# Kernel optimization log

Hardware: AMD Instinct MI355X
Metric: run time of the kernel (lower is better)

## Reference

```python
import jax, jax.numpy as jnp
import numpy as np

N, CIN, CH, W = 512, 128, 256, 8

def _refpad(x):
    # ReflectionPad2d(1) on NCHW
    return jnp.pad(x, ((0, 0), (0, 0), (1, 1), (1, 1)), mode='reflect')

def _conv(x, w, b):
    # x: NCHW padded, w: OIHW 3x3, VALID conv back to 8x8
    y = jax.lax.conv_general_dilated(x, w, (1, 1), 'VALID',
                                     dimension_numbers=('NCHW', 'OIHW', 'NCHW'))
    return y + b[None, :, None, None]

def setup_inputs() -> dict:
    key = jax.random.key(0)
    ks = jax.random.split(key, 24)
    s_in = 1.0 / np.sqrt(CIN * 9)
    s_h = 1.0 / np.sqrt(CH * 9)
    d = {
        'x': jax.random.normal(ks[0], (N, CIN, W, W), jnp.float32),
        'hidden_state': jax.random.normal(ks[1], (N, 2, CH, W, W), jnp.float32),
    }
    names_i = ['w_ii', 'w_if', 'w_ig', 'w_io']
    names_h = ['w_hi', 'w_hf', 'w_hg', 'w_ho']
    for j, nm in enumerate(names_i):
        d[nm] = jax.random.uniform(ks[2 + j], (CH, CIN, 3, 3), jnp.float32, -s_in, s_in)
        d[nm.replace('w_', 'b_')] = jax.random.uniform(ks[6 + j], (CH,), jnp.float32, -s_in, s_in)
    for j, nm in enumerate(names_h):
        d[nm] = jax.random.uniform(ks[10 + j], (CH, CH, 3, 3), jnp.float32, -s_h, s_h)
        d[nm.replace('w_', 'b_')] = jax.random.uniform(ks[14 + j], (CH,), jnp.float32, -s_h, s_h)
    # peephole weights: initialized to zeros in the original module
    d['wc_i'] = jnp.zeros((1, CH, W, W), jnp.float32)
    d['wc_f'] = jnp.zeros((1, CH, W, W), jnp.float32)
    d['wc_o'] = jnp.zeros((1, CH, W, W), jnp.float32)
    return d

def reference(x, hidden_state, w_ii, b_ii, w_if, b_if, w_ig, b_ig, w_io, b_io,
              w_hi, b_hi, w_hf, b_hf, w_hg, b_hg, w_ho, b_ho, wc_i, wc_f, wc_o):
    h0 = hidden_state[:, 0]  # (N, CH, 8, 8)
    c0 = hidden_state[:, 1]
    xp = _refpad(x)
    hp = _refpad(h0)
    # Fuse the 4 input-side convs and 4 hidden-side convs into one conv each
    wi = jnp.concatenate([w_ii, w_if, w_ig, w_io], axis=0)
    bi = jnp.concatenate([b_ii, b_if, b_ig, b_io], axis=0)
    wh = jnp.concatenate([w_hi, w_hf, w_hg, w_ho], axis=0)
    bh = jnp.concatenate([b_hi, b_hf, b_hg, b_ho], axis=0)
    gates = _conv(xp, wi, bi) + _conv(hp, wh, bh)  # (N, 4*CH, 8, 8)
    gi, gf, gg, go = jnp.split(gates, 4, axis=1)
    i = jax.nn.sigmoid(gi + c0 * wc_i)
    f = jax.nn.sigmoid(gf + c0 * wc_f)
    g = jnp.tanh(gg)
    c_t = c0 + f * c0 + i * g
    o = jax.nn.sigmoid(go + c_t * wc_o)
    h_t = h0 + o * jnp.tanh(c_t)
    hidden_state_out = jnp.stack([h_t, c_t], axis=1)  # (N, 2, CH, 8, 8)
    return o, hidden_state_out
```

## Files before the change

### kernel.cpp

```cpp
#include <hip/hip_runtime.h>
#include <hip/hip_bf16.h>

typedef __bf16 bf16x8 __attribute__((ext_vector_type(8)));
typedef float  f32x4  __attribute__((ext_vector_type(4)));

#define RSX 136
#define RSH 264

#define BCHT 221184

__device__ __forceinline__ ushort f2bf(float f) {
    union { float f; uint i; } c; c.f = f;
    uint u = c.i;
    u = (u + 0x7fff + ((u >> 16) & 1)) >> 16;
    return (ushort)u;
}
__device__ __forceinline__ float sigmoidf_(float x) {
    x = fminf(fmaxf(x, -30.0f), 30.0f);
    return 1.0f / (1.0f + expf(-x));
}
__device__ __forceinline__ float tanhf_(float x) {
    x = fminf(fmaxf(x, -15.0f), 15.0f);
    const float e = expf(-2.0f * x);
    return (1.0f - e) / (1.0f + e);
}

__global__ void prep_wt(const float* __restrict__ wii, const float* __restrict__ wif,
                        const float* __restrict__ wig, const float* __restrict__ wio,
                        const float* __restrict__ whi, const float* __restrict__ whf,
                        const float* __restrict__ whg, const float* __restrict__ who,
                        ushort* __restrict__ Wt) {
    const int idx = blockIdx.x * 256 + threadIdx.x;
    if (idx < 131072) {
        const int g   = idx >> 15;
        const int rem = idx & 32767;
        const int ch  = rem >> 7, ic = rem & 127;
        const float* w = (g == 0) ? wii : (g == 1) ? wif : (g == 2) ? wig : wio;
        const float* src = w + (size_t)(ch * 128 + ic) * 9;
        const int cht = ch >> 4, lm = ch & 15;
        ushort* dst = Wt + (size_t)cht * BCHT + g * 512 + lm * 8;
        #pragma unroll
        for (int s = 0; s < 9; ++s) {
            const int k = s * 128 + ic;
            const int chunk = k >> 5, kg = (k >> 3) & 3, ke = k & 7;
            dst[chunk * 2048 + kg * 128 + ke] = f2bf(src[s]);
        }
    } else {
        const int j   = idx - 131072;
        const int g   = j >> 16;
        const int rem = j & 65535;
        const int ch  = rem >> 8, ic = rem & 255;
        const float* w = (g == 0) ? whi : (g == 1) ? whf : (g == 2) ? whg : who;
        const float* src = w + (size_t)(ch * 256 + ic) * 9;
        const int cht = ch >> 4, lm = ch & 15;
        ushort* dst = Wt + (size_t)cht * BCHT + g * 512 + lm * 8;
        #pragma unroll
        for (int s = 0; s < 9; ++s) {
            const int k = 1152 + s * 256 + ic;
            const int chunk = k >> 5, kg = (k >> 3) & 3, ke = k & 7;
            dst[chunk * 2048 + kg * 128 + ke] = f2bf(src[s]);
        }
    }
}

__global__ void prep_bias(const float* __restrict__ bii, const float* __restrict__ bif,
                          const float* __restrict__ big, const float* __restrict__ bio,
                          const float* __restrict__ bhi, const float* __restrict__ bhf,
                          const float* __restrict__ bhg, const float* __restrict__ bho,
                          float* __restrict__ btot) {
    const int g = blockIdx.x, ch = threadIdx.x;
    const float* bi = (g == 0) ? bii : (g == 1) ? bif : (g == 2) ? big : bio;
    const float* bh = (g == 0) ? bhi : (g == 1) ? bhf : (g == 2) ? bhg : bho;
    btot[g * 256 + ch] = bi[ch] + bh[ch];
}

__global__ __launch_bounds__(256, 4)
void convlstm_main(const float* __restrict__ x, const float* __restrict__ hidden,
                   const ushort* __restrict__ Wt, const float* __restrict__ btot,
                   const float* __restrict__ wci, const float* __restrict__ wcf,
                   const float* __restrict__ wco, float* __restrict__ out) {
    __shared__ alignas(16) ushort lds[64 * RSH];

    const int octile = blockIdx.x;
    const int img    = blockIdx.y;
    const int tid    = threadIdx.x;
    const int lane   = tid & 63;
    const int wave   = tid >> 6;
    const int lm     = lane & 15;
    const int kg     = lane >> 4;

    f32x4 acc[4][4];
    #pragma unroll
    for (int ms = 0; ms < 4; ++ms)
        #pragma unroll
        for (int ns = 0; ns < 4; ++ns)
            #pragma unroll
            for (int r = 0; r < 4; ++r) acc[ms][ns][r] = 0.0f;

    const ushort* Bw = Wt + (size_t)(octile * 4 + wave) * BCHT + (size_t)lane * 8;

    {
        const float* xs = x + img * 8192;
        #pragma unroll
        for (int it = 0; it < 4; ++it) {
            const int icp = lane;
            const int p0  = (it * 4 + wave) * 4;
            const float4 f0 = *(const float4*)(xs + (2 * icp    ) * 64 + p0);
            const float4 f1 = *(const float4*)(xs + (2 * icp + 1) * 64 + p0);
            const float a0[4] = {f0.x, f0.y, f0.z, f0.w};
            const float a1[4] = {f1.x, f1.y, f1.z, f1.w};
            #pragma unroll
            for (int j = 0; j < 4; ++j) {
                const uint pk = (uint)f2bf(a0[j]) | ((uint)f2bf(a1[j]) << 16);
                *(uint*)(&lds[(p0 + j) * RSX + 2 * icp]) = pk;
            }
        }
    }
    __syncthreads();

    #pragma unroll 1
    for (int seg = 0; seg < 9; ++seg) {
        const int dy = seg / 3 - 1, dx = seg % 3 - 1;
        int aoff[4];
        #pragma unroll
        for (int ms = 0; ms < 4; ++ms) {
            const int pm = ms * 16 + lm;
            const int yy = pm >> 3, xx = pm & 7;
            int sy = yy + dy; sy = (sy < 0) ? 1 : ((sy > 7) ? 6 : sy);
            int sx = xx + dx; sx = (sx < 0) ? 1 : ((sx > 7) ? 6 : sx);
            aoff[ms] = (sy * 8 + sx) * RSX + kg * 8;
        }
        #pragma unroll
        for (int ic0 = 0; ic0 < 128; ic0 += 32) {
            const int c = seg * 4 + (ic0 >> 5);
            const ushort* Bc = Bw + (size_t)c * 2048;
            bf16x8 a[4], b[4];
            #pragma unroll
            for (int ms = 0; ms < 4; ++ms) a[ms] = *(const bf16x8*)(&lds[aoff[ms] + ic0]);
            #pragma unroll
            for (int ns = 0; ns < 4; ++ns) b[ns] = *(const bf16x8*)(Bc + ns * 512);
            #pragma unroll
            for (int ms = 0; ms < 4; ++ms)
                #pragma unroll
                for (int ns = 0; ns < 4; ++ns)
                    acc[ms][ns] = __builtin_amdgcn_mfma_f32_16x16x32_bf16(a[ms], b[ns], acc[ms][ns], 0, 0, 0);
        }
    }

    __syncthreads();
    {
        const float* hs = hidden + img * 32768;
        #pragma unroll
        for (int it = 0; it < 8; ++it) {
            const int icp = (it & 1) * 64 + lane;
            const int p0  = ((it >> 1) * 4 + wave) * 4;
            const float4 f0 = *(const float4*)(hs + (2 * icp    ) * 64 + p0);
            const float4 f1 = *(const float4*)(hs + (2 * icp + 1) * 64 + p0);
            const float a0[4] = {f0.x, f0.y, f0.z, f0.w};
            const float a1[4] = {f1.x, f1.y, f1.z, f1.w};
            #pragma unroll
            for (int j = 0; j < 4; ++j) {
                const uint pk = (uint)f2bf(a0[j]) | ((uint)f2bf(a1[j]) << 16);
                *(uint*)(&lds[(p0 + j) * RSH + 2 * icp]) = pk;
            }
        }
    }
    __syncthreads();

    #pragma unroll 1
    for (int seg = 0; seg < 9; ++seg) {
        const int dy = seg / 3 - 1, dx = seg % 3 - 1;
        int aoff[4];
        #pragma unroll
        for (int ms = 0; ms < 4; ++ms) {
            const int pm = ms * 16 + lm;
            const int yy = pm >> 3, xx = pm & 7;
            int sy = yy + dy; sy = (sy < 0) ? 1 : ((sy > 7) ? 6 : sy);
            int sx = xx + dx; sx = (sx < 0) ? 1 : ((sx > 7) ? 6 : sx);
            aoff[ms] = (sy * 8 + sx) * RSH + kg * 8;
        }
        #pragma unroll
        for (int ic0 = 0; ic0 < 256; ic0 += 32) {
            const int c = 36 + seg * 8 + (ic0 >> 5);
            const ushort* Bc = Bw + (size_t)c * 2048;
            bf16x8 a[4], b[4];
            #pragma unroll
            for (int ms = 0; ms < 4; ++ms) a[ms] = *(const bf16x8*)(&lds[aoff[ms] + ic0]);
            #pragma unroll
            for (int ns = 0; ns < 4; ++ns) b[ns] = *(const bf16x8*)(Bc + ns * 512);
            #pragma unroll
            for (int ms = 0; ms < 4; ++ms)
                #pragma unroll
                for (int ns = 0; ns < 4; ++ns)
                    acc[ms][ns] = __builtin_amdgcn_mfma_f32_16x16x32_bf16(a[ms], b[ns], acc[ms][ns], 0, 0, 0);
        }
    }

    const int ch   = (octile * 4 + wave) * 16 + lm;
    const int quad = lane >> 4;

    const float* h0p = hidden + img * 32768 + ch * 64;
    const float* c0p = h0p + 16384;
    const float* wip = wci + ch * 64;
    const float* wfp = wcf + ch * 64;
    const float* wop = wco + ch * 64;
    const float bi_ = btot[      ch];
    const float bf_ = btot[256 + ch];
    const float bg_ = btot[512 + ch];
    const float bo_ = btot[768 + ch];

    float* o_out = out + img * 16384 + ch * 64;
    float* h_out = out + 8388608 + img * 32768 + ch * 64;
    float* c_out = h_out + 16384;

    #pragma unroll
    for (int ms = 0; ms < 4; ++ms) {
        const int P0 = ms * 16 + quad * 4;
        union { float4 v; float f[4]; } c0u, h0u, wiu, wfu, wou, ov4, hv4, cv4;
        c0u.v = *(const float4*)(c0p + P0);
        h0u.v = *(const float4*)(h0p + P0);
        wiu.v = *(const float4*)(wip + P0);
        wfu.v = *(const float4*)(wfp + P0);
        wou.v = *(const float4*)(wop + P0);
        #pragma unroll
        for (int r = 0; r < 4; ++r) {
            const float c0v = c0u.f[r];
            const float h0v = h0u.f[r];
            const float gi = acc[ms][0][r] + bi_;
            const float gf = acc[ms][1][r] + bf_;
            const float gg = acc[ms][2][r] + bg_;
            const float go = acc[ms][3][r] + bo_;
            const float iv = sigmoidf_(gi + c0v * wiu.f[r]);
            const float fv = sigmoidf_(gf + c0v * wfu.f[r]);
            const float gv = tanhf_(gg);
            const float ct = c0v + fv * c0v + iv * gv;
            const float ov = sigmoidf_(go + ct * wou.f[r]);
            const float ht = h0v + ov * tanhf_(ct);
            ov4.f[r] = ov;
            hv4.f[r] = ht;
            cv4.f[r] = ct;
        }
        *(float4*)(o_out + P0) = ov4.v;
        *(float4*)(h_out + P0) = hv4.v;
        *(float4*)(c_out + P0) = cv4.v;
    }
}

extern "C" void kernel_launch(void* const* d_in, const int* in_sizes, int n_in,
                              void* d_out, int out_size, void* d_ws, size_t ws_size,
                              hipStream_t stream) {
    const float* x      = (const float*)d_in[0];
    const float* hidden = (const float*)d_in[1];
    const float* wii = (const float*)d_in[2];  const float* bii = (const float*)d_in[3];
    const float* wif = (const float*)d_in[4];  const float* bif = (const float*)d_in[5];
    const float* wig = (const float*)d_in[6];  const float* big = (const float*)d_in[7];
    const float* wio = (const float*)d_in[8];  const float* bio = (const float*)d_in[9];
    const float* whi = (const float*)d_in[10]; const float* bhi = (const float*)d_in[11];
    const float* whf = (const float*)d_in[12]; const float* bhf = (const float*)d_in[13];
    const float* whg = (const float*)d_in[14]; const float* bhg = (const float*)d_in[15];
    const float* who = (const float*)d_in[16]; const float* bho = (const float*)d_in[17];
    const float* wci = (const float*)d_in[18];
    const float* wcf = (const float*)d_in[19];
    const float* wco = (const float*)d_in[20];

    ushort* Wt  = (ushort*)d_ws;
    float* btot = (float*)((char*)d_ws + (size_t)16 * BCHT * 2);

    prep_wt<<<dim3(1536), 256, 0, stream>>>(wii, wif, wig, wio, whi, whf, whg, who, Wt);
    prep_bias<<<dim3(4), 256, 0, stream>>>(bii, bif, big, bio, bhi, bhf, bhg, bho, btot);
    convlstm_main<<<dim3(4, 512), 256, 0, stream>>>(x, hidden, Wt, btot, wci, wcf, wco,
                                                    (float*)d_out);
}
```

Before: 434.5 us.

## Process two images per block to reuse weight loads, rotate tap order

Each block now computes two images, so every weight fragment loaded from global memory feeds MFMAs for both images. This halves weight traffic per image. The accumulator count doubles to 128 floats per lane and LDS grows to two hidden images, so launch bounds drop to 2 blocks per CU and the grid halves. The starting conv tap is also rotated per image pair so that concurrent blocks read different weight chunks and spread cache access.

```diff
diff --git a/kernel.cpp b/kernel.cpp
--- a/kernel.cpp
+++ b/kernel.cpp
@@ -6,6 +6,8 @@
 
 #define RSX 136
 #define RSH 264
+#define XIMG (64 * RSX)
+#define HIMG (64 * RSH)
 
 #define BCHT 221184
 
@@ -74,33 +76,37 @@
     btot[g * 256 + ch] = bi[ch] + bh[ch];
 }
 
-__global__ __launch_bounds__(256, 4)
+__global__ __launch_bounds__(256, 2)
 void convlstm_main(const float* __restrict__ x, const float* __restrict__ hidden,
                    const ushort* __restrict__ Wt, const float* __restrict__ btot,
                    const float* __restrict__ wci, const float* __restrict__ wcf,
                    const float* __restrict__ wco, float* __restrict__ out) {
-    __shared__ alignas(16) ushort lds[64 * RSH];
+    __shared__ alignas(16) ushort lds[2 * HIMG];
 
     const int octile = blockIdx.x;
-    const int img    = blockIdx.y;
+    const int ipair  = blockIdx.y;
     const int tid    = threadIdx.x;
     const int lane   = tid & 63;
     const int wave   = tid >> 6;
     const int lm     = lane & 15;
     const int kg     = lane >> 4;
-
-    f32x4 acc[4][4];
-    #pragma unroll
-    for (int ms = 0; ms < 4; ++ms)
-        #pragma unroll
-        for (int ns = 0; ns < 4; ++ns)
-            #pragma unroll
-            for (int r = 0; r < 4; ++r) acc[ms][ns][r] = 0.0f;
+    const int rot    = ipair % 9;
+
+    f32x4 acc[2][4][4];
+    #pragma unroll
+    for (int im = 0; im < 2; ++im)
+        #pragma unroll
+        for (int ms = 0; ms < 4; ++ms)
+            #pragma unroll
+            for (int ns = 0; ns < 4; ++ns)
+                #pragma unroll
+                for (int r = 0; r < 4; ++r) acc[im][ms][ns][r] = 0.0f;
 
     const ushort* Bw = Wt + (size_t)(octile * 4 + wave) * BCHT + (size_t)lane * 8;
 
-    {
-        const float* xs = x + img * 8192;
+    #pragma unroll
+    for (int im = 0; im < 2; ++im) {
+        const float* xs = x + (size_t)(2 * ipair + im) * 8192;
         #pragma unroll
         for (int it = 0; it < 4; ++it) {
             const int icp = lane;
@@ -112,14 +118,15 @@
             #pragma unroll
             for (int j = 0; j < 4; ++j) {
                 const uint pk = (uint)f2bf(a0[j]) | ((uint)f2bf(a1[j]) << 16);
-                *(uint*)(&lds[(p0 + j) * RSX + 2 * icp]) = pk;
+                *(uint*)(&lds[im * XIMG + (p0 + j) * RSX + 2 * icp]) = pk;
             }
         }
     }
     __syncthreads();
 
     #pragma unroll 1
-    for (int seg = 0; seg < 9; ++seg) {
+    for (int ss = 0; ss < 9; ++ss) {
+        int seg = ss + rot; if (seg >= 9) seg -= 9;
         const int dy = seg / 3 - 1, dx = seg % 3 - 1;
         int aoff[4];
         #pragma unroll
@@ -134,22 +141,29 @@
         for (int ic0 = 0; ic0 < 128; ic0 += 32) {
             const int c = seg * 4 + (ic0 >> 5);
             const ushort* Bc = Bw + (size_t)c * 2048;
-            bf16x8 a[4], b[4];
-            #pragma unroll
-            for (int ms = 0; ms < 4; ++ms) a[ms] = *(const bf16x8*)(&lds[aoff[ms] + ic0]);
+            bf16x8 b[4];
             #pragma unroll
             for (int ns = 0; ns < 4; ++ns) b[ns] = *(const bf16x8*)(Bc + ns * 512);
             #pragma unroll
-            for (int ms = 0; ms < 4; ++ms)
-                #pragma unroll
-                for (int ns = 0; ns < 4; ++ns)
-                    acc[ms][ns] = __builtin_amdgcn_mfma_f32_16x16x32_bf16(a[ms], b[ns], acc[ms][ns], 0, 0, 0);
+            for (int im = 0; im < 2; ++im) {
+                bf16x8 a[4];
+                #pragma unroll
+                for (int ms = 0; ms < 4; ++ms)
+                    a[ms] = *(const bf16x8*)(&lds[im * XIMG + aoff[ms] + ic0]);
+                #pragma unroll
+                for (int ms = 0; ms < 4; ++ms)
+                    #pragma unroll
+                    for (int ns = 0; ns < 4; ++ns)
+                        acc[im][ms][ns] = __builtin_amdgcn_mfma_f32_16x16x32_bf16(
+                            a[ms], b[ns], acc[im][ms][ns], 0, 0, 0);
+            }
         }
     }
 
     __syncthreads();
-    {
-        const float* hs = hidden + img * 32768;
+    #pragma unroll
+    for (int im = 0; im < 2; ++im) {
+        const float* hs = hidden + (size_t)(2 * ipair + im) * 32768;
         #pragma unroll
         for (int it = 0; it < 8; ++it) {
             const int icp = (it & 1) * 64 + lane;
@@ -161,14 +175,15 @@
             #pragma unroll
             for (int j = 0; j < 4; ++j) {
                 const uint pk = (uint)f2bf(a0[j]) | ((uint)f2bf(a1[j]) << 16);
-                *(uint*)(&lds[(p0 + j) * RSH + 2 * icp]) = pk;
+                *(uint*)(&lds[im * HIMG + (p0 + j) * RSH + 2 * icp]) = pk;
             }
         }
     }
     __syncthreads();
 
     #pragma unroll 1
-    for (int seg = 0; seg < 9; ++seg) {
+    for (int ss = 0; ss < 9; ++ss) {
+        int seg = ss + rot; if (seg >= 9) seg -= 9;
         const int dy = seg / 3 - 1, dx = seg % 3 - 1;
         int aoff[4];
         #pragma unroll
@@ -183,66 +198,75 @@
         for (int ic0 = 0; ic0 < 256; ic0 += 32) {
             const int c = 36 + seg * 8 + (ic0 >> 5);
             const ushort* Bc = Bw + (size_t)c * 2048;
-            bf16x8 a[4], b[4];
-            #pragma unroll
-            for (int ms = 0; ms < 4; ++ms) a[ms] = *(const bf16x8*)(&lds[aoff[ms] + ic0]);
+            bf16x8 b[4];
             #pragma unroll
             for (int ns = 0; ns < 4; ++ns) b[ns] = *(const bf16x8*)(Bc + ns * 512);
             #pragma unroll
-            for (int ms = 0; ms < 4; ++ms)
-                #pragma unroll
-                for (int ns = 0; ns < 4; ++ns)
-                    acc[ms][ns] = __builtin_amdgcn_mfma_f32_16x16x32_bf16(a[ms], b[ns], acc[ms][ns], 0, 0, 0);
+            for (int im = 0; im < 2; ++im) {
+                bf16x8 a[4];
+                #pragma unroll
+                for (int ms = 0; ms < 4; ++ms)
+                    a[ms] = *(const bf16x8*)(&lds[im * HIMG + aoff[ms] + ic0]);
+                #pragma unroll
+                for (int ms = 0; ms < 4; ++ms)
+                    #pragma unroll
+                    for (int ns = 0; ns < 4; ++ns)
+                        acc[im][ms][ns] = __builtin_amdgcn_mfma_f32_16x16x32_bf16(
+                            a[ms], b[ns], acc[im][ms][ns], 0, 0, 0);
+            }
         }
     }
 
     const int ch   = (octile * 4 + wave) * 16 + lm;
     const int quad = lane >> 4;
-
-    const float* h0p = hidden + img * 32768 + ch * 64;
-    const float* c0p = h0p + 16384;
-    const float* wip = wci + ch * 64;
-    const float* wfp = wcf + ch * 64;
-    const float* wop = wco + ch * 64;
     const float bi_ = btot[      ch];
     const float bf_ = btot[256 + ch];
     const float bg_ = btot[512 + ch];
     const float bo_ = btot[768 + ch];
-
-    float* o_out = out + img * 16384 + ch * 64;
-    float* h_out = out + 8388608 + img * 32768 + ch * 64;
-    float* c_out = h_out + 16384;
-
-    #pragma unroll
-    for (int ms = 0; ms < 4; ++ms) {
-        const int P0 = ms * 16 + quad * 4;
-        union { float4 v; float f[4]; } c0u, h0u, wiu, wfu, wou, ov4, hv4, cv4;
-        c0u.v = *(const float4*)(c0p + P0);
-        h0u.v = *(const float4*)(h0p + P0);
-        wiu.v = *(const float4*)(wip + P0);
-        wfu.v = *(const float4*)(wfp + P0);
-        wou.v = *(const float4*)(wop + P0);
-        #pragma unroll
-        for (int r = 0; r < 4; ++r) {
-            const float c0v = c0u.f[r];
-            const float h0v = h0u.f[r];
-            const float gi = acc[ms][0][r] + bi_;
-            const float gf = acc[ms][1][r] + bf_;
-            const float gg = acc[ms][2][r] + bg_;
-            const float go = acc[ms][3][r] + bo_;
-            const float iv = sigmoidf_(gi + c0v * wiu.f[r]);
-            const float fv = sigmoidf_(gf + c0v * wfu.f[r]);
-            const float gv = tanhf_(gg);
-            const float ct = c0v + fv * c0v + iv * gv;
-            const float ov = sigmoidf_(go + ct * wou.f[r]);
-            const float ht = h0v + ov * tanhf_(ct);
-            ov4.f[r] = ov;
-            hv4.f[r] = ht;
-            cv4.f[r] = ct;
-        }
-        *(float4*)(o_out + P0) = ov4.v;
-        *(float4*)(h_out + P0) = hv4.v;
-        *(float4*)(c_out + P0) = cv4.v;
+    const float* wip = wci + ch * 64;
+    const float* wfp = wcf + ch * 64;
+    const float* wop = wco + ch * 64;
+
+    #pragma unroll
+    for (int im = 0; im < 2; ++im) {
+        const int img = 2 * ipair + im;
+        const float* h0p = hidden + (size_t)img * 32768 + ch * 64;
+        const float* c0p = h0p + 16384;
+        float* o_out = out + (size_t)img * 16384 + ch * 64;
+        float* h_out = out + 8388608 + (size_t)img * 32768 + ch * 64;
+        float* c_out = h_out + 16384;
+
+        #pragma unroll
+        for (int ms = 0; ms < 4; ++ms) {
+            const int P0 = ms * 16 + quad * 4;
+            union { float4 v; float f[4]; } c0u, h0u, wiu, wfu, wou, ov4, hv4, cv4;
+            c0u.v = *(const float4*)(c0p + P0);
+            h0u.v = *(const float4*)(h0p + P0);
+            wiu.v = *(const float4*)(wip + P0);
+            wfu.v = *(const float4*)(wfp + P0);
+            wou.v = *(const float4*)(wop + P0);
+            #pragma unroll
+            for (int r = 0; r < 4; ++r) {
+                const float c0v = c0u.f[r];
+                const float h0v = h0u.f[r];
+                const float gi = acc[im][ms][0][r] + bi_;
+                const float gf = acc[im][ms][1][r] + bf_;
+                const float gg = acc[im][ms][2][r] + bg_;
+                const float go = acc[im][ms][3][r] + bo_;
+                const float iv = sigmoidf_(gi + c0v * wiu.f[r]);
+                const float fv = sigmoidf_(gf + c0v * wfu.f[r]);
+                const float gv = tanhf_(gg);
+                const float ct = c0v + fv * c0v + iv * gv;
+                const float ov = sigmoidf_(go + ct * wou.f[r]);
+                const float ht = h0v + ov * tanhf_(ct);
+                ov4.f[r] = ov;
+                hv4.f[r] = ht;
+                cv4.f[r] = ct;
+            }
+            *(float4*)(o_out + P0) = ov4.v;
+            *(float4*)(h_out + P0) = hv4.v;
+            *(float4*)(c_out + P0) = cv4.v;
+        }
     }
 }
 
@@ -268,6 +292,6 @@
 
     prep_wt<<<dim3(1536), 256, 0, stream>>>(wii, wif, wig, wio, whi, whf, whg, who, Wt);
     prep_bias<<<dim3(4), 256, 0, stream>>>(bii, bif, big, bio, bhi, bhf, bhg, bho, btot);
-    convlstm_main<<<dim3(4, 512), 256, 0, stream>>>(x, hidden, Wt, btot, wci, wcf, wco,
+    convlstm_main<<<dim3(4, 256), 256, 0, stream>>>(x, hidden, Wt, btot, wci, wcf, wco,
                                                     (float*)d_out);
 }
```

New measurement: 424.0 us. 2.4% less time.

## Software-pipeline weight fragment loads with inline-asm prefetch and manual vmcnt waits

Applied to the files above, without the earlier changes.

Weight fragments are now prefetched four K-chunks ahead into a rotating register buffer, using inline-asm global_load_dwordx4 and explicit s_waitcnt vmcnt(12) plus scheduling barriers before each MFMA group. This is meant to hide global and L2 latency on the B operand behind the MFMA work, where before each chunk was loaded and consumed in the same step. Launch bounds drop from 4 to 2 waves per EU so the extra live registers fit. That costs occupancy, and hand-managed vmcnt counting that the compiler cannot see is fragile.

```diff
diff --git a/kernel.cpp b/kernel.cpp
--- a/kernel.cpp
+++ b/kernel.cpp
@@ -3,6 +3,7 @@
 
 typedef __bf16 bf16x8 __attribute__((ext_vector_type(8)));
 typedef float  f32x4  __attribute__((ext_vector_type(4)));
+typedef int    i32x4  __attribute__((ext_vector_type(4)));
 
 #define RSX 136
 #define RSH 264
@@ -14,6 +15,9 @@
     uint u = c.i;
     u = (u + 0x7fff + ((u >> 16) & 1)) >> 16;
     return (ushort)u;
+}
+__device__ __forceinline__ bf16x8 as_bf16x8(i32x4 v) {
+    union { i32x4 i; bf16x8 b; } u; u.i = v; return u.b;
 }
 __device__ __forceinline__ float sigmoidf_(float x) {
     x = fminf(fmaxf(x, -30.0f), 30.0f);
@@ -74,7 +78,17 @@
     btot[g * 256 + ch] = bi[ch] + bh[ch];
 }
 
-__global__ __launch_bounds__(256, 4)
+#define BLOAD4(buf, cidx) do {                                               \
+    const unsigned long long _p = (unsigned long long)(Bw + (size_t)(cidx) * 2048); \
+    asm volatile("global_load_dwordx4 %0, %1, off"             : "=&v"(buf[0]) : "v"(_p)); \
+    asm volatile("global_load_dwordx4 %0, %1, off offset:1024" : "=&v"(buf[1]) : "v"(_p)); \
+    asm volatile("global_load_dwordx4 %0, %1, off offset:2048" : "=&v"(buf[2]) : "v"(_p)); \
+    asm volatile("global_load_dwordx4 %0, %1, off offset:3072" : "=&v"(buf[3]) : "v"(_p)); \
+} while (0)
+
+#define WAITB(n) asm volatile("s_waitcnt vmcnt(" #n ")" ::: "memory")
+
+__global__ __launch_bounds__(256, 2)
 void convlstm_main(const float* __restrict__ x, const float* __restrict__ hidden,
                    const ushort* __restrict__ Wt, const float* __restrict__ btot,
                    const float* __restrict__ wci, const float* __restrict__ wcf,
@@ -99,6 +113,12 @@
 
     const ushort* Bw = Wt + (size_t)(octile * 4 + wave) * BCHT + (size_t)lane * 8;
 
+    i32x4 bb[4][4];
+    BLOAD4(bb[0], 0);
+    BLOAD4(bb[1], 1);
+    BLOAD4(bb[2], 2);
+    BLOAD4(bb[3], 3);
+
     {
         const float* xs = x + img * 8192;
         #pragma unroll
@@ -131,19 +151,21 @@
             aoff[ms] = (sy * 8 + sx) * RSX + kg * 8;
         }
         #pragma unroll
-        for (int ic0 = 0; ic0 < 128; ic0 += 32) {
-            const int c = seg * 4 + (ic0 >> 5);
-            const ushort* Bc = Bw + (size_t)c * 2048;
-            bf16x8 a[4], b[4];
+        for (int i = 0; i < 4; ++i) {
+            const int ic0 = i * 32;
+            bf16x8 a[4];
             #pragma unroll
             for (int ms = 0; ms < 4; ++ms) a[ms] = *(const bf16x8*)(&lds[aoff[ms] + ic0]);
-            #pragma unroll
-            for (int ns = 0; ns < 4; ++ns) b[ns] = *(const bf16x8*)(Bc + ns * 512);
+            WAITB(12);
+            __builtin_amdgcn_sched_barrier(0);
             #pragma unroll
             for (int ms = 0; ms < 4; ++ms)
                 #pragma unroll
                 for (int ns = 0; ns < 4; ++ns)
-                    acc[ms][ns] = __builtin_amdgcn_mfma_f32_16x16x32_bf16(a[ms], b[ns], acc[ms][ns], 0, 0, 0);
+                    acc[ms][ns] = __builtin_amdgcn_mfma_f32_16x16x32_bf16(
+                        a[ms], as_bf16x8(bb[i][ns]), acc[ms][ns], 0, 0, 0);
+            int cn = seg * 4 + i + 4; if (cn > 107) cn = 107;
+            BLOAD4(bb[i], cn);
         }
     }
 
@@ -180,21 +202,27 @@
             aoff[ms] = (sy * 8 + sx) * RSH + kg * 8;
         }
         #pragma unroll
-        for (int ic0 = 0; ic0 < 256; ic0 += 32) {
-            const int c = 36 + seg * 8 + (ic0 >> 5);
-            const ushort* Bc = Bw + (size_t)c * 2048;
-            bf16x8 a[4], b[4];
+        for (int i = 0; i < 8; ++i) {
+            const int ic0 = i * 32;
+            bf16x8 a[4];
             #pragma unroll
             for (int ms = 0; ms < 4; ++ms) a[ms] = *(const bf16x8*)(&lds[aoff[ms] + ic0]);
-            #pragma unroll
-            for (int ns = 0; ns < 4; ++ns) b[ns] = *(const bf16x8*)(Bc + ns * 512);
+            WAITB(12);
+            __builtin_amdgcn_sched_barrier(0);
             #pragma unroll
             for (int ms = 0; ms < 4; ++ms)
                 #pragma unroll
                 for (int ns = 0; ns < 4; ++ns)
-                    acc[ms][ns] = __builtin_amdgcn_mfma_f32_16x16x32_bf16(a[ms], b[ns], acc[ms][ns], 0, 0, 0);
-        }
-    }
+                    acc[ms][ns] = __builtin_amdgcn_mfma_f32_16x16x32_bf16(
+                        a[ms], as_bf16x8(bb[i & 3][ns]), acc[ms][ns], 0, 0, 0);
+            int cn = 36 + seg * 8 + i + 4; if (cn > 107) cn = 107;
+            BLOAD4(bb[i & 3], cn);
+        }
+    }
+
+    __builtin_amdgcn_sched_barrier(0);
+    WAITB(0);
+    __builtin_amdgcn_sched_barrier(0);
 
     const int ch   = (octile * 4 + wave) * 16 + lm;
     const int quad = lane >> 4;
```

After: 409.9 us. -5.7%, faster.

## Switch conv GEMM to 32x32x16 MFMA with repacked weights and shuffled epilogue

Applied to the files above, without the earlier changes.

Replaces the 16x16x32 bf16 MFMA tiling (4x4 accumulators) with 32x32x16 MFMA (2x2 accumulators). Weights are repacked so that each 32-column B tile interleaves two gates for 16 channels. Gate values are exchanged between lane halves with shuffles in the epilogue, and each half writes a different output. The aim is fewer MFMA issues and fewer LDS and global operand loads per FLOP. In exchange, the epilogue does redundant activation math on both lane halves and launch bounds drop to 3 blocks per CU, with s_setprio added around the MFMA bursts.

```diff
diff --git a/kernel.cpp b/kernel.cpp
--- a/kernel.cpp
+++ b/kernel.cpp
@@ -1,8 +1,9 @@
 #include <hip/hip_runtime.h>
 #include <hip/hip_bf16.h>
 
-typedef __bf16 bf16x8 __attribute__((ext_vector_type(8)));
-typedef float  f32x4  __attribute__((ext_vector_type(4)));
+typedef __bf16 bf16x8  __attribute__((ext_vector_type(8)));
+typedef float  f32x4   __attribute__((ext_vector_type(4)));
+typedef float  f32x16  __attribute__((ext_vector_type(16)));
 
 #define RSX 136
 #define RSH 264
@@ -37,28 +38,30 @@
         const int ch  = rem >> 7, ic = rem & 127;
         const float* w = (g == 0) ? wii : (g == 1) ? wif : (g == 2) ? wig : wio;
         const float* src = w + (size_t)(ch * 128 + ic) * 9;
-        const int cht = ch >> 4, lm = ch & 15;
-        ushort* dst = Wt + (size_t)cht * BCHT + g * 512 + lm * 8;
+        const int cht = ch >> 4;
+        const int c   = ((g & 1) << 4) | (ch & 15);
+        ushort* dst = Wt + (size_t)cht * BCHT + (g >> 1) * 512 + c * 8;
         #pragma unroll
         for (int s = 0; s < 9; ++s) {
             const int k = s * 128 + ic;
-            const int chunk = k >> 5, kg = (k >> 3) & 3, ke = k & 7;
-            dst[chunk * 2048 + kg * 128 + ke] = f2bf(src[s]);
+            const int chunk = k >> 5, kstep = (k >> 4) & 1, lh = (k >> 3) & 1, j = k & 7;
+            dst[chunk * 2048 + kstep * 1024 + lh * 256 + j] = f2bf(src[s]);
         }
     } else {
-        const int j   = idx - 131072;
-        const int g   = j >> 16;
-        const int rem = j & 65535;
+        const int jj  = idx - 131072;
+        const int g   = jj >> 16;
+        const int rem = jj & 65535;
         const int ch  = rem >> 8, ic = rem & 255;
         const float* w = (g == 0) ? whi : (g == 1) ? whf : (g == 2) ? whg : who;
         const float* src = w + (size_t)(ch * 256 + ic) * 9;
-        const int cht = ch >> 4, lm = ch & 15;
-        ushort* dst = Wt + (size_t)cht * BCHT + g * 512 + lm * 8;
+        const int cht = ch >> 4;
+        const int c   = ((g & 1) << 4) | (ch & 15);
+        ushort* dst = Wt + (size_t)cht * BCHT + (g >> 1) * 512 + c * 8;
         #pragma unroll
         for (int s = 0; s < 9; ++s) {
             const int k = 1152 + s * 256 + ic;
-            const int chunk = k >> 5, kg = (k >> 3) & 3, ke = k & 7;
-            dst[chunk * 2048 + kg * 128 + ke] = f2bf(src[s]);
+            const int chunk = k >> 5, kstep = (k >> 4) & 1, lh = (k >> 3) & 1, j = k & 7;
+            dst[chunk * 2048 + kstep * 1024 + lh * 256 + j] = f2bf(src[s]);
         }
     }
 }
@@ -74,7 +77,9 @@
     btot[g * 256 + ch] = bi[ch] + bh[ch];
 }
 
-__global__ __launch_bounds__(256, 4)
+#define MFMA32(A, B, C) __builtin_amdgcn_mfma_f32_32x32x16_bf16((A), (B), (C), 0, 0, 0)
+
+__global__ __launch_bounds__(256, 3)
 void convlstm_main(const float* __restrict__ x, const float* __restrict__ hidden,
                    const ushort* __restrict__ Wt, const float* __restrict__ btot,
                    const float* __restrict__ wci, const float* __restrict__ wcf,
@@ -86,16 +91,16 @@
     const int tid    = threadIdx.x;
     const int lane   = tid & 63;
     const int wave   = tid >> 6;
-    const int lm     = lane & 15;
-    const int kg     = lane >> 4;
-
-    f32x4 acc[4][4];
+    const int l31    = lane & 31;
+    const int lh8    = (lane >> 5) * 8;
+
+    f32x16 acc[2][2];
     #pragma unroll
-    for (int ms = 0; ms < 4; ++ms)
-        #pragma unroll
-        for (int ns = 0; ns < 4; ++ns)
+    for (int m = 0; m < 2; ++m)
+        #pragma unroll
+        for (int n = 0; n < 2; ++n)
             #pragma unroll
-            for (int r = 0; r < 4; ++r) acc[ms][ns][r] = 0.0f;
+            for (int r = 0; r < 16; ++r) acc[m][n][r] = 0.0f;
 
     const ushort* Bw = Wt + (size_t)(octile * 4 + wave) * BCHT + (size_t)lane * 8;
 
@@ -121,29 +126,37 @@
     #pragma unroll 1
     for (int seg = 0; seg < 9; ++seg) {
         const int dy = seg / 3 - 1, dx = seg % 3 - 1;
-        int aoff[4];
-        #pragma unroll
-        for (int ms = 0; ms < 4; ++ms) {
-            const int pm = ms * 16 + lm;
-            const int yy = pm >> 3, xx = pm & 7;
+        int aoff[2];
+        #pragma unroll
+        for (int m = 0; m < 2; ++m) {
+            const int px = m * 32 + l31;
+            const int yy = px >> 3, xx = px & 7;
             int sy = yy + dy; sy = (sy < 0) ? 1 : ((sy > 7) ? 6 : sy);
             int sx = xx + dx; sx = (sx < 0) ? 1 : ((sx > 7) ? 6 : sx);
-            aoff[ms] = (sy * 8 + sx) * RSX + kg * 8;
-        }
-        #pragma unroll
-        for (int ic0 = 0; ic0 < 128; ic0 += 32) {
-            const int c = seg * 4 + (ic0 >> 5);
-            const ushort* Bc = Bw + (size_t)c * 2048;
-            bf16x8 a[4], b[4];
-            #pragma unroll
-            for (int ms = 0; ms < 4; ++ms) a[ms] = *(const bf16x8*)(&lds[aoff[ms] + ic0]);
-            #pragma unroll
-            for (int ns = 0; ns < 4; ++ns) b[ns] = *(const bf16x8*)(Bc + ns * 512);
-            #pragma unroll
-            for (int ms = 0; ms < 4; ++ms)
-                #pragma unroll
-                for (int ns = 0; ns < 4; ++ns)
-                    acc[ms][ns] = __builtin_amdgcn_mfma_f32_16x16x32_bf16(a[ms], b[ns], acc[ms][ns], 0, 0, 0);
+            aoff[m] = (sy * 8 + sx) * RSX + lh8;
+        }
+        #pragma unroll
+        for (int i = 0; i < 4; ++i) {
+            const int ic0 = i * 32;
+            const ushort* Bc = Bw + (size_t)(seg * 4 + i) * 2048;
+            const bf16x8 a0k0 = *(const bf16x8*)(&lds[aoff[0] + ic0]);
+            const bf16x8 a0k1 = *(const bf16x8*)(&lds[aoff[0] + ic0 + 16]);
+            const bf16x8 a1k0 = *(const bf16x8*)(&lds[aoff[1] + ic0]);
+            const bf16x8 a1k1 = *(const bf16x8*)(&lds[aoff[1] + ic0 + 16]);
+            const bf16x8 b00 = *(const bf16x8*)(Bc);
+            const bf16x8 b01 = *(const bf16x8*)(Bc + 512);
+            const bf16x8 b10 = *(const bf16x8*)(Bc + 1024);
+            const bf16x8 b11 = *(const bf16x8*)(Bc + 1536);
+            __builtin_amdgcn_s_setprio(1);
+            acc[0][0] = MFMA32(a0k0, b00, acc[0][0]);
+            acc[0][1] = MFMA32(a0k0, b01, acc[0][1]);
+            acc[1][0] = MFMA32(a1k0, b00, acc[1][0]);
+            acc[1][1] = MFMA32(a1k0, b01, acc[1][1]);
+            acc[0][0] = MFMA32(a0k1, b10, acc[0][0]);
+            acc[0][1] = MFMA32(a0k1, b11, acc[0][1]);
+            acc[1][0] = MFMA32(a1k1, b10, acc[1][0]);
+            acc[1][1] = MFMA32(a1k1, b11, acc[1][1]);
+            __builtin_amdgcn_s_setprio(0);
         }
     }
 
@@ -170,34 +183,44 @@
     #pragma unroll 1
     for (int seg = 0; seg < 9; ++seg) {
         const int dy = seg / 3 - 1, dx = seg % 3 - 1;
-        int aoff[4];
-        #pragma unroll
-        for (int ms = 0; ms < 4; ++ms) {
-            const int pm = ms * 16 + lm;
-            const int yy = pm >> 3, xx = pm & 7;
+        int aoff[2];
+        #pragma unroll
+        for (int m = 0; m < 2; ++m) {
+            const int px = m * 32 + l31;
+            const int yy = px >> 3, xx = px & 7;
             int sy = yy + dy; sy = (sy < 0) ? 1 : ((sy > 7) ? 6 : sy);
             int sx = xx + dx; sx = (sx < 0) ? 1 : ((sx > 7) ? 6 : sx);
-            aoff[ms] = (sy * 8 + sx) * RSH + kg * 8;
-        }
-        #pragma unroll
-        for (int ic0 = 0; ic0 < 256; ic0 += 32) {
-            const int c = 36 + seg * 8 + (ic0 >> 5);
-            const ushort* Bc = Bw + (size_t)c * 2048;
-            bf16x8 a[4], b[4];
-            #pragma unroll
-            for (int ms = 0; ms < 4; ++ms) a[ms] = *(const bf16x8*)(&lds[aoff[ms] + ic0]);
-            #pragma unroll
-            for (int ns = 0; ns < 4; ++ns) b[ns] = *(const bf16x8*)(Bc + ns * 512);
-            #pragma unroll
-            for (int ms = 0; ms < 4; ++ms)
-                #pragma unroll
-                for (int ns = 0; ns < 4; ++ns)
-                    acc[ms][ns] = __builtin_amdgcn_mfma_f32_16x16x32_bf16(a[ms], b[ns], acc[ms][ns], 0, 0, 0);
-        }
-    }
-
-    const int ch   = (octile * 4 + wave) * 16 + lm;
-    const int quad = lane >> 4;
+            aoff[m] = (sy * 8 + sx) * RSH + lh8;
+        }
+        #pragma unroll
+        for (int i = 0; i < 8; ++i) {
+            const int ic0 = i * 32;
+            const ushort* Bc = Bw + (size_t)(36 + seg * 8 + i) * 2048;
+            const bf16x8 a0k0 = *(const bf16x8*)(&lds[aoff[0] + ic0]);
+            const bf16x8 a0k1 = *(const bf16x8*)(&lds[aoff[0] + ic0 + 16]);
+            const bf16x8 a1k0 = *(const bf16x8*)(&lds[aoff[1] + ic0]);
+            const bf16x8 a1k1 = *(const bf16x8*)(&lds[aoff[1] + ic0 + 16]);
+            const bf16x8 b00 = *(const bf16x8*)(Bc);
+            const bf16x8 b01 = *(const bf16x8*)(Bc + 512);
+            const bf16x8 b10 = *(const bf16x8*)(Bc + 1024);
+            const bf16x8 b11 = *(const bf16x8*)(Bc + 1536);
+            __builtin_amdgcn_s_setprio(1);
+            acc[0][0] = MFMA32(a0k0, b00, acc[0][0]);
+            acc[0][1] = MFMA32(a0k0, b01, acc[0][1]);
+            acc[1][0] = MFMA32(a1k0, b00, acc[1][0]);
+            acc[1][1] = MFMA32(a1k0, b01, acc[1][1]);
+            acc[0][0] = MFMA32(a0k1, b10, acc[0][0]);
+            acc[0][1] = MFMA32(a0k1, b11, acc[0][1]);
+            acc[1][0] = MFMA32(a1k1, b10, acc[1][0]);
+            acc[1][1] = MFMA32(a1k1, b11, acc[1][1]);
+            __builtin_amdgcn_s_setprio(0);
+        }
+    }
+
+    const int oc = l31 & 15;
+    const int ga = l31 >> 4;
+    const int hi = lane >> 5;
+    const int ch = (octile * 4 + wave) * 16 + oc;
 
     const float* h0p = hidden + img * 32768 + ch * 64;
     const float* c0p = h0p + 16384;
@@ -214,35 +237,45 @@
     float* c_out = h_out + 16384;
 
     #pragma unroll
-    for (int ms = 0; ms < 4; ++ms) {
-        const int P0 = ms * 16 + quad * 4;
-        union { float4 v; float f[4]; } c0u, h0u, wiu, wfu, wou, ov4, hv4, cv4;
-        c0u.v = *(const float4*)(c0p + P0);
-        h0u.v = *(const float4*)(h0p + P0);
-        wiu.v = *(const float4*)(wip + P0);
-        wfu.v = *(const float4*)(wfp + P0);
-        wou.v = *(const float4*)(wop + P0);
-        #pragma unroll
-        for (int r = 0; r < 4; ++r) {
-            const float c0v = c0u.f[r];
-            const float h0v = h0u.f[r];
-            const float gi = acc[ms][0][r] + bi_;
-            const float gf = acc[ms][1][r] + bf_;
-            const float gg = acc[ms][2][r] + bg_;
-            const float go = acc[ms][3][r] + bo_;
-            const float iv = sigmoidf_(gi + c0v * wiu.f[r]);
-            const float fv = sigmoidf_(gf + c0v * wfu.f[r]);
-            const float gv = tanhf_(gg);
-            const float ct = c0v + fv * c0v + iv * gv;
-            const float ov = sigmoidf_(go + ct * wou.f[r]);
-            const float ht = h0v + ov * tanhf_(ct);
-            ov4.f[r] = ov;
-            hv4.f[r] = ht;
-            cv4.f[r] = ct;
-        }
-        *(float4*)(o_out + P0) = ov4.v;
-        *(float4*)(h_out + P0) = hv4.v;
-        *(float4*)(c_out + P0) = cv4.v;
+    for (int m = 0; m < 2; ++m) {
+        #pragma unroll
+        for (int q = 0; q < 4; ++q) {
+            const int P0 = m * 32 + q * 8 + hi * 4;
+            union { float4 v; float f[4]; } c0u, h0u, wiu, wfu, wou, ov4, hv4, cv4;
+            c0u.v = *(const float4*)(c0p + P0);
+            h0u.v = *(const float4*)(h0p + P0);
+            wiu.v = *(const float4*)(wip + P0);
+            wfu.v = *(const float4*)(wfp + P0);
+            wou.v = *(const float4*)(wop + P0);
+            #pragma unroll
+            for (int r = 0; r < 4; ++r) {
+                const float own0 = acc[m][0][q * 4 + r];
+                const float own1 = acc[m][1][q * 4 + r];
+                const float rec0 = __shfl_xor(own0, 16, 64);
+                const float rec1 = __shfl_xor(own1, 16, 64);
+                const float gi = (ga ? rec0 : own0) + bi_;
+                const float gf = (ga ? own0 : rec0) + bf_;
+                const float gg = (ga ? rec1 : own1) + bg_;
+                const float go = (ga ? own1 : rec1) + bo_;
+                const float c0v = c0u.f[r];
+                const float h0v = h0u.f[r];
+                const float iv = sigmoidf_(gi + c0v * wiu.f[r]);
+                const float fv = sigmoidf_(gf + c0v * wfu.f[r]);
+                const float gv = tanhf_(gg);
+                const float ct = c0v + fv * c0v + iv * gv;
+                const float ov = sigmoidf_(go + ct * wou.f[r]);
+                const float ht = h0v + ov * tanhf_(ct);
+                ov4.f[r] = ov;
+                hv4.f[r] = ht;
+                cv4.f[r] = ct;
+            }
+            if (ga == 0) {
+                *(float4*)(o_out + P0) = ov4.v;
+                *(float4*)(h_out + P0) = hv4.v;
+            } else {
+                *(float4*)(c_out + P0) = cv4.v;
+            }
+        }
     }
 }
 
```

Result: slower. 466.1 us (+7.3%).
